# Kernel tuning notes

Measured on AMD Instinct MI355X. Metric: run time of the kernel, lower is better.

Reference implementation:

```python
import jax, jax.numpy as jnp
import numpy as np
from jax import lax

B, K, L = 8, 64, 1024
CP, AP, G2 = 32, 8, 9
CSA, ASA, G3 = 16, 16, 3
ROUT_ITER = 3
EPS = 1e-08


def squash(s):
    sq = jnp.sum(s * s, axis=-1, keepdims=True)
    return sq / (1.0 + sq) * (s / jnp.sqrt(sq + EPS))


def routing(V, iters):
    # V: [B, L, cp, cSA, aSA]
    b = jnp.zeros(V.shape[:-1], dtype=V.dtype)  # [B, L, cp, cSA]
    v = None
    for r in range(iters):
        c = jax.nn.softmax(b, axis=-1)[..., None]          # [B,L,cp,cSA,1]
        s = jnp.sum(c * V, axis=-3)                        # [B,L,cSA,aSA]
        v = squash(s)
        if r < iters - 1:
            a = jnp.sum(V * v[..., None, :, :], axis=-1)   # [B,L,cp,cSA]
            b = b + lax.stop_gradient(a)
    return v


def setup_inputs() -> dict:
    key = jax.random.key(0)
    k1, k2, k3 = jax.random.split(key, 3)
    x = jax.random.normal(k1, (B, K, L), dtype=jnp.float32)
    w1 = jax.random.normal(k2, (CP * AP, K, G2), dtype=jnp.float32) * 0.05
    b1 = jnp.zeros((CP * AP,), dtype=jnp.float32)
    w2 = jax.random.normal(k3, (CSA * ASA, 1, G3, AP), dtype=jnp.float32) * 0.05
    b2 = jnp.zeros((CSA * ASA,), dtype=jnp.float32)
    return {"x": x, "w1": w1, "b1": b1, "w2": w2, "b2": b2}


def reference(x, w1, b1, w2, b2):
    # conv1: Conv1d(k -> cp*ap, kernel g2, padding 'same')
    y = lax.conv_general_dilated(x, w1, window_strides=(1,), padding='SAME',
                                 dimension_numbers=('NCH', 'OIH', 'NCH'))
    y = y + b1[None, :, None]                              # [B, cp*ap, L]
    y = jnp.transpose(y, (0, 2, 1)).reshape(B, L, CP, AP)
    y = squash(y)
    y = y.reshape(B, L, CP * AP)[:, None]                  # [B, 1, L, cp*ap]
    # conv2: Conv2d(1 -> cSA*aSA, kernel (g3, ap), stride (1, ap), pad ((g3-1)/2, 0))
    pad = (G3 - 1) // 2
    z = lax.conv_general_dilated(y, w2, window_strides=(1, AP),
                                 padding=((pad, pad), (0, 0)),
                                 dimension_numbers=('NCHW', 'OIHW', 'NCHW'))
    z = z + b2[None, :, None, None]                        # [B, cSA*aSA, L, cp]
    V = jnp.transpose(z, (0, 2, 3, 1)).reshape(B, L, CP, CSA, ASA)
    v = routing(V, ROUT_ITER)                              # [B, L, cSA, aSA]
    return v.reshape(B, L * CSA, ASA)
```

## Files before the change

kernel.cpp:

```cpp
#include <hip/hip_runtime.h>
#include <math.h>

#define NB   8
#define NK   64
#define NL   1024
#define NCP  32
#define NAP  8
#define NG2  9
#define NCSA 16
#define NASA 16
#define NG3  3
#define NOC  256
#define EPSQ 1e-8f
#define VROW 129

typedef __bf16 bfv8 __attribute__((ext_vector_type(8)));
typedef float  f32x4 __attribute__((ext_vector_type(4)));

static __device__ inline unsigned short bfbits(float v) {
    __bf16 h = (__bf16)v;
    return __builtin_bit_cast(unsigned short, h);
}
static __device__ inline unsigned int bfpack2(float v0, float v1) {
    return (unsigned int)bfbits(v0) | ((unsigned int)bfbits(v1) << 16);
}
static __device__ inline float frcp(float x) { return __builtin_amdgcn_rcpf(x); }
static __device__ inline float frsq(float x) { return __builtin_amdgcn_rsqf(x); }

__global__ __launch_bounds__(256) void k0_prep(
    const float* __restrict__ x, const float* __restrict__ w1,
    const float* __restrict__ w2,
    __bf16* __restrict__ xThi, __bf16* __restrict__ w1Thi,
    __bf16* __restrict__ w2hi)
{
    const int tid = threadIdx.x;
    const int bid = blockIdx.x;
    if (bid < 128) {
        __shared__ float tile[64][65];
        const int b = bid >> 4, l0 = (bid & 15) * 64;
        const float* xb = x + (size_t)b * NK * NL;
        const int lcol = tid & 63, kr = tid >> 6;
#pragma unroll
        for (int pass = 0; pass < 16; ++pass) {
            int kk = pass * 4 + kr;
            tile[lcol][kk] = xb[(size_t)kk * NL + l0 + lcol];
        }
        __syncthreads();
        const int lr = tid >> 5, pc = tid & 31;
#pragma unroll
        for (int pass = 0; pass < 8; ++pass) {
            int ll = pass * 8 + lr;
            float v0 = tile[ll][pc * 2], v1 = tile[ll][pc * 2 + 1];
            size_t base = ((size_t)b * NL + l0 + ll) * 64 + pc * 2;
            *(unsigned int*)(xThi + base) = bfpack2(v0, v1);
        }
    } else if (bid < 128 + 288) {
        int idx = (bid - 128) * 256 + tid;
        int kp = idx & 31, rest = idx >> 5;
        int oc = rest & 255, g = rest >> 8;
        float v0 = w1[(size_t)oc * 576 + (kp * 2) * NG2 + g];
        float v1 = w1[(size_t)oc * 576 + (kp * 2 + 1) * NG2 + g];
        size_t base = ((size_t)(g * NOC + oc)) * 64 + kp * 2;
        *(unsigned int*)(w1Thi + base) = bfpack2(v0, v1);
    } else {
        for (int i = tid; i < NOC * 24; i += 256) {
            w2hi[i] = (__bf16)w2[i];
        }
    }
}

__global__ __launch_bounds__(256) void k1_mfma(
    const __bf16* __restrict__ xThi, const __bf16* __restrict__ w1Thi,
    const float* __restrict__ b1, __bf16* __restrict__ ysq)
{
    __shared__ alignas(16) __bf16 xph[72][64];
    const int tid = threadIdx.x;
    const int bid = blockIdx.x;
    const int ocb = bid & 3;
    const int lb  = (bid >> 2) & 15;
    const int b   = bid >> 6;
    const int l0  = lb * 64;

    {
        const int row0 = tid >> 3, seg = tid & 7;
#pragma unroll
        for (int p = 0; p < 3; ++p) {
            int row = p * 32 + row0;
            if (row < 72) {
                int l = l0 - 4 + row;
                int sw = seg ^ (row & 7);
                uint4 vh = {0u,0u,0u,0u};
                if (l >= 0 && l < NL) {
                    size_t off = ((size_t)b * NL + l) * 64 + seg * 8;
                    vh = *(const uint4*)(xThi + off);
                }
                *(uint4*)(&xph[row][sw * 8]) = vh;
            }
        }
    }
    __syncthreads();

    const int lane = tid & 63, wv = tid >> 6;
    const int qq = lane >> 4, cr = lane & 15;
    const int oco = ocb * 64 + wv * 16;

    f32x4 acc[4];
#pragma unroll
    for (int lt = 0; lt < 4; ++lt) acc[lt] = (f32x4){0.f, 0.f, 0.f, 0.f};

    for (int g = 0; g < NG2; ++g) {
#pragma unroll
        for (int s = 0; s < 2; ++s) {
            size_t aoff = ((size_t)(g * NOC + oco + cr)) * 64 + s * 32 + qq * 8;
            bfv8 Ahi = *(const bfv8*)(w1Thi + aoff);
#pragma unroll
            for (int lt = 0; lt < 4; ++lt) {
                int row = lt * 16 + cr + g;
                int gr = (s * 4 + qq) ^ (row & 7);
                bfv8 Bhi = *(const bfv8*)(&xph[row][gr * 8]);
                acc[lt] = __builtin_amdgcn_mfma_f32_16x16x32_bf16(Ahi, Bhi, acc[lt], 0, 0, 0);
            }
        }
    }

    const float4 bv = *(const float4*)(b1 + oco + qq * 4);
#pragma unroll
    for (int lt = 0; lt < 4; ++lt) {
        float v0 = acc[lt][0] + bv.x, v1 = acc[lt][1] + bv.y;
        float v2 = acc[lt][2] + bv.z, v3 = acc[lt][3] + bv.w;
        float s = v0*v0 + v1*v1 + v2*v2 + v3*v3;
        float s8 = s + __shfl_xor(s, 16);
        float scale = s8 * frcp(1.0f + s8) * frsq(s8 + EPSQ);
        uint2 st;
        st.x = bfpack2(v0 * scale, v1 * scale);
        st.y = bfpack2(v2 * scale, v3 * scale);
        int l = l0 + lt * 16 + cr;
        *(uint2*)(ysq + ((size_t)b * NL + l) * NOC + oco + qq * 4) = st;
    }
}

__global__ __launch_bounds__(256, 4) void k2_conv2_routing(
    const __bf16* __restrict__ ysq,
    const __bf16* __restrict__ w2hi,
    const float* __restrict__ b2, float* __restrict__ out)
{
    __shared__ alignas(16) unsigned int VbW[NCP * VROW];
    __shared__ alignas(16) float cct[NCSA][36];
    __shared__ alignas(16) float vvs[NCSA][20];

    const int tid = threadIdx.x;
    const int bid = blockIdx.x;
    const int b = bid >> 10;
    const int l = bid & (NL - 1);

    const int lane = tid & 63;
    const int wv   = tid >> 6;
    const int q    = lane >> 4;
    const int cr   = lane & 15;

    const __bf16* ybase = ysq + ((size_t)b * NL + l) * NOC;
    const bool rowok = (q == 1) || (q == 0 && l > 0) || (q == 2 && l < NL - 1);
    bfv8 B0, B1;
    if (rowok) {
        B0 = *(const bfv8*)(ybase + (q - 1) * NOC + cr * 8);
        B1 = *(const bfv8*)(ybase + (q - 1) * NOC + (cr + 16) * 8);
    } else {
#pragma unroll
        for (int i = 0; i < 8; ++i) { B0[i] = (__bf16)0.0f; B1[i] = (__bf16)0.0f; }
    }

    const int swz0 = (cr & 3) << 3;
#pragma unroll
    for (int i = 0; i < 4; ++i) {
        const int t  = wv * 4 + i;
        const int oc = t * 16 + cr;
        bfv8 Ahi;
        if (q < 3) {
            Ahi = *(const bfv8*)(w2hi + oc * 24 + q * 8);
        } else {
#pragma unroll
            for (int j = 0; j < 8; ++j) Ahi[j] = (__bf16)0.0f;
        }

        f32x4 acc0 = {0.f, 0.f, 0.f, 0.f};
        f32x4 acc1 = {0.f, 0.f, 0.f, 0.f};
        acc0 = __builtin_amdgcn_mfma_f32_16x16x32_bf16(Ahi, B0, acc0, 0, 0, 0);
        acc1 = __builtin_amdgcn_mfma_f32_16x16x32_bf16(Ahi, B1, acc1, 0, 0, 0);

        const int r0 = t * 16 + q * 4;
        float4 bvv = *(const float4*)(b2 + r0);
        const int D = t * 8 + q * 2;
        const int d0 = D ^ swz0;
        VbW[cr * VROW + d0]            = bfpack2(acc0[0] + bvv.x, acc0[1] + bvv.y);
        VbW[cr * VROW + d0 + 1]        = bfpack2(acc0[2] + bvv.z, acc0[3] + bvv.w);
        VbW[(cr + 16) * VROW + d0]     = bfpack2(acc1[0] + bvv.x, acc1[1] + bvv.y);
        VbW[(cr + 16) * VROW + d0 + 1] = bfpack2(acc1[2] + bvv.z, acc1[3] + bvv.w);
    }
    __syncthreads();

    const int csa = tid >> 4, asa = tid & 15;
    const int cp8 = tid >> 3, cs = tid & 7;

    const __bf16* vbB = (const __bf16*)VbW;
    float Vreg[NCP];
    {
        const int tw = tid >> 1, th = tid & 1;
#pragma unroll
        for (int cp = 0; cp < NCP; ++cp) {
            int d = tw ^ ((cp & 3) << 3);
            Vreg[cp] = (float)vbB[cp * (2 * VROW) + d * 2 + th];
        }
    }

    unsigned int ar0[8], ar1[8];
    {
        const unsigned int* arow0 = VbW + cp8 * VROW + ((cs * 8) ^ ((cp8 & 3) << 3));
        const unsigned int* arow1 = VbW + cp8 * VROW + (((cs + 8) * 8) ^ ((cp8 & 3) << 3));
#pragma unroll
        for (int j = 0; j < 8; ++j) { ar0[j] = arow0[j]; ar1[j] = arow1[j]; }
    }

    float br0, br1;

    {
        float s0 = 0.f, s1 = 0.f, s2 = 0.f, s3 = 0.f;
#pragma unroll
        for (int cp = 0; cp < NCP; cp += 4) {
            s0 += Vreg[cp];     s1 += Vreg[cp + 1];
            s2 += Vreg[cp + 2]; s3 += Vreg[cp + 3];
        }
        float sv = ((s0 + s1) + (s2 + s3)) * 0.0625f;
        float sq = sv * sv;
        sq += __shfl_xor(sq, 1);
        sq += __shfl_xor(sq, 2);
        sq += __shfl_xor(sq, 4);
        sq += __shfl_xor(sq, 8);
        float vval = sv * sq * frcp(1.0f + sq) * frsq(sq + EPSQ);
        vvs[csa][asa] = vval;
        __syncthreads();

        float4 va[4], vb[4];
#pragma unroll
        for (int p = 0; p < 4; ++p) {
            va[p] = ((const float4*)(&vvs[cs][0]))[p];
            vb[p] = ((const float4*)(&vvs[cs + 8][0]))[p];
        }
        float a0a = 0.f, a0b = 0.f, a1a = 0.f, a1b = 0.f;
#pragma unroll
        for (int j = 0; j < 8; ++j) {
            unsigned int d0 = ar0[j], d1 = ar1[j];
            float ve0 = (j & 1) ? va[j >> 1].z : va[j >> 1].x;
            float vo0 = (j & 1) ? va[j >> 1].w : va[j >> 1].y;
            float ve1 = (j & 1) ? vb[j >> 1].z : vb[j >> 1].x;
            float vo1 = (j & 1) ? vb[j >> 1].w : vb[j >> 1].y;
            a0a = fmaf(__builtin_bit_cast(float, d0 << 16),          ve0, a0a);
            a0b = fmaf(__builtin_bit_cast(float, d0 & 0xFFFF0000u),  vo0, a0b);
            a1a = fmaf(__builtin_bit_cast(float, d1 << 16),          ve1, a1a);
            a1b = fmaf(__builtin_bit_cast(float, d1 & 0xFFFF0000u),  vo1, a1b);
        }
        br0 = a0a + a0b;
        br1 = a1a + a1b;
    }

    {
        float e0 = __expf(br0), e1 = __expf(br1);
        float ssum = e0 + e1;
        ssum += __shfl_xor(ssum, 1);
        ssum += __shfl_xor(ssum, 2);
        ssum += __shfl_xor(ssum, 4);
        float inv = frcp(ssum);
        cct[cs][cp8]     = e0 * inv;
        cct[cs + 8][cp8] = e1 * inv;
        __syncthreads();

        float s0 = 0.f, s1 = 0.f, s2 = 0.f, s3 = 0.f;
        const float4* ccrow = (const float4*)(&cct[csa][0]);
#pragma unroll
        for (int jj = 0; jj < 8; ++jj) {
            float4 c4 = ccrow[jj];
            s0 = fmaf(c4.x, Vreg[4 * jj + 0], s0);
            s1 = fmaf(c4.y, Vreg[4 * jj + 1], s1);
            s2 = fmaf(c4.z, Vreg[4 * jj + 2], s2);
            s3 = fmaf(c4.w, Vreg[4 * jj + 3], s3);
        }
        float sv = (s0 + s1) + (s2 + s3);
        float sq = sv * sv;
        sq += __shfl_xor(sq, 1);
        sq += __shfl_xor(sq, 2);
        sq += __shfl_xor(sq, 4);
        sq += __shfl_xor(sq, 8);
        float vval = sv * sq * frcp(1.0f + sq) * frsq(sq + EPSQ);
        vvs[csa][asa] = vval;
        __syncthreads();

        float4 va[4], vb[4];
#pragma unroll
        for (int p = 0; p < 4; ++p) {
            va[p] = ((const float4*)(&vvs[cs][0]))[p];
            vb[p] = ((const float4*)(&vvs[cs + 8][0]))[p];
        }
        float a0a = 0.f, a0b = 0.f, a1a = 0.f, a1b = 0.f;
#pragma unroll
        for (int j = 0; j < 8; ++j) {
            unsigned int d0 = ar0[j], d1 = ar1[j];
            float ve0 = (j & 1) ? va[j >> 1].z : va[j >> 1].x;
            float vo0 = (j & 1) ? va[j >> 1].w : va[j >> 1].y;
            float ve1 = (j & 1) ? vb[j >> 1].z : vb[j >> 1].x;
            float vo1 = (j & 1) ? vb[j >> 1].w : vb[j >> 1].y;
            a0a = fmaf(__builtin_bit_cast(float, d0 << 16),          ve0, a0a);
            a0b = fmaf(__builtin_bit_cast(float, d0 & 0xFFFF0000u),  vo0, a0b);
            a1a = fmaf(__builtin_bit_cast(float, d1 << 16),          ve1, a1a);
            a1b = fmaf(__builtin_bit_cast(float, d1 & 0xFFFF0000u),  vo1, a1b);
        }
        br0 += a0a + a0b;
        br1 += a1a + a1b;
    }

    {
        float e0 = __expf(br0), e1 = __expf(br1);
        float ssum = e0 + e1;
        ssum += __shfl_xor(ssum, 1);
        ssum += __shfl_xor(ssum, 2);
        ssum += __shfl_xor(ssum, 4);
        float inv = frcp(ssum);
        cct[cs][cp8]     = e0 * inv;
        cct[cs + 8][cp8] = e1 * inv;
        __syncthreads();

        float s0 = 0.f, s1 = 0.f, s2 = 0.f, s3 = 0.f;
        const float4* ccrow = (const float4*)(&cct[csa][0]);
#pragma unroll
        for (int jj = 0; jj < 8; ++jj) {
            float4 c4 = ccrow[jj];
            s0 = fmaf(c4.x, Vreg[4 * jj + 0], s0);
            s1 = fmaf(c4.y, Vreg[4 * jj + 1], s1);
            s2 = fmaf(c4.z, Vreg[4 * jj + 2], s2);
            s3 = fmaf(c4.w, Vreg[4 * jj + 3], s3);
        }
        float sv = (s0 + s1) + (s2 + s3);
        float sq = sv * sv;
        sq += __shfl_xor(sq, 1);
        sq += __shfl_xor(sq, 2);
        sq += __shfl_xor(sq, 4);
        sq += __shfl_xor(sq, 8);
        float vval = sv * sq * frcp(1.0f + sq) * frsq(sq + EPSQ);
        out[((size_t)b * NL + l) * NOC + tid] = vval;
    }
}

extern "C" void kernel_launch(void* const* d_in, const int* in_sizes, int n_in,
                              void* d_out, int out_size, void* d_ws, size_t ws_size,
                              hipStream_t stream)
{
    const float* x  = (const float*)d_in[0];
    const float* w1 = (const float*)d_in[1];
    const float* b1 = (const float*)d_in[2];
    const float* w2 = (const float*)d_in[3];
    const float* b2 = (const float*)d_in[4];
    float* outp = (float*)d_out;

    char* ws = (char*)d_ws;
    __bf16* ysq   = (__bf16*)(ws);
    __bf16* xThi  = (__bf16*)(ws + 4194304);
    __bf16* w1Thi = (__bf16*)(ws + 5242880);
    __bf16* w2hi  = (__bf16*)(ws + 5537792);

    k0_prep<<<417, 256, 0, stream>>>(x, w1, w2, xThi, w1Thi, w2hi);
    k1_mfma<<<512, 256, 0, stream>>>(xThi, w1Thi, b1, ysq);
    k2_conv2_routing<<<NB * NL, 256, 0, stream>>>(ysq, w2hi, b2, outp);
}
```

Baseline: 54.45 us.

## Process two sequence positions per block in conv2+routing kernel

Each block of the conv2/routing kernel now handles two adjacent positions, doubling the MFMA, routing and shared-memory work per block and halving the grid. This amortises the weight loads, bias loads and barrier count across two independent routing problems and gives more ILP between barriers. The agreement loads now read shared memory directly instead of caching rows in registers. Launch bounds drop to 2 blocks per CU because of the higher register and LDS use, which risks lower occupancy.

```diff
diff --git a/kernel.cpp b/kernel.cpp
--- a/kernel.cpp
+++ b/kernel.cpp
@@ -139,34 +139,47 @@
     }
 }
 
-__global__ __launch_bounds__(256, 4) void k2_conv2_routing(
+__global__ __launch_bounds__(256, 2) void k2_conv2_routing(
     const __bf16* __restrict__ ysq,
     const __bf16* __restrict__ w2hi,
     const float* __restrict__ b2, float* __restrict__ out)
 {
-    __shared__ alignas(16) unsigned int VbW[NCP * VROW];
-    __shared__ alignas(16) float cct[NCSA][36];
-    __shared__ alignas(16) float vvs[NCSA][20];
+    __shared__ alignas(16) unsigned int VbWA[NCP * VROW];
+    __shared__ alignas(16) unsigned int VbWB[NCP * VROW];
+    __shared__ alignas(16) float cctA[NCSA][36];
+    __shared__ alignas(16) float cctB[NCSA][36];
+    __shared__ alignas(16) float vvsA[NCSA][20];
+    __shared__ alignas(16) float vvsB[NCSA][20];
 
     const int tid = threadIdx.x;
     const int bid = blockIdx.x;
-    const int b = bid >> 10;
-    const int l = bid & (NL - 1);
+    const int b  = bid >> 9;
+    const int lA = (bid & 511) * 2;
+    const int lB = lA + 1;
 
     const int lane = tid & 63;
     const int wv   = tid >> 6;
     const int q    = lane >> 4;
     const int cr   = lane & 15;
 
-    const __bf16* ybase = ysq + ((size_t)b * NL + l) * NOC;
-    const bool rowok = (q == 1) || (q == 0 && l > 0) || (q == 2 && l < NL - 1);
-    bfv8 B0, B1;
-    if (rowok) {
-        B0 = *(const bfv8*)(ybase + (q - 1) * NOC + cr * 8);
-        B1 = *(const bfv8*)(ybase + (q - 1) * NOC + (cr + 16) * 8);
+    const __bf16* ybaseA = ysq + ((size_t)b * NL + lA) * NOC;
+    const __bf16* ybaseB = ybaseA + NOC;
+    const bool okA = (q == 1) || (q == 0 && lA > 0) || (q == 2);
+    const bool okB = (q == 1) || (q == 0) || (q == 2 && lB < NL - 1);
+    bfv8 B0A, B1A, B0B, B1B;
+    if (okA) {
+        B0A = *(const bfv8*)(ybaseA + (q - 1) * NOC + cr * 8);
+        B1A = *(const bfv8*)(ybaseA + (q - 1) * NOC + (cr + 16) * 8);
     } else {
 #pragma unroll
-        for (int i = 0; i < 8; ++i) { B0[i] = (__bf16)0.0f; B1[i] = (__bf16)0.0f; }
+        for (int i = 0; i < 8; ++i) { B0A[i] = (__bf16)0.0f; B1A[i] = (__bf16)0.0f; }
+    }
+    if (okB) {
+        B0B = *(const bfv8*)(ybaseB + (q - 1) * NOC + cr * 8);
+        B1B = *(const bfv8*)(ybaseB + (q - 1) * NOC + (cr + 16) * 8);
+    } else {
+#pragma unroll
+        for (int i = 0; i < 8; ++i) { B0B[i] = (__bf16)0.0f; B1B[i] = (__bf16)0.0f; }
     }
 
     const int swz0 = (cr & 3) << 3;
@@ -182,169 +195,188 @@
             for (int j = 0; j < 8; ++j) Ahi[j] = (__bf16)0.0f;
         }
 
-        f32x4 acc0 = {0.f, 0.f, 0.f, 0.f};
-        f32x4 acc1 = {0.f, 0.f, 0.f, 0.f};
-        acc0 = __builtin_amdgcn_mfma_f32_16x16x32_bf16(Ahi, B0, acc0, 0, 0, 0);
-        acc1 = __builtin_amdgcn_mfma_f32_16x16x32_bf16(Ahi, B1, acc1, 0, 0, 0);
+        f32x4 aA0 = {0.f,0.f,0.f,0.f}, aA1 = {0.f,0.f,0.f,0.f};
+        f32x4 aB0 = {0.f,0.f,0.f,0.f}, aB1 = {0.f,0.f,0.f,0.f};
+        aA0 = __builtin_amdgcn_mfma_f32_16x16x32_bf16(Ahi, B0A, aA0, 0, 0, 0);
+        aA1 = __builtin_amdgcn_mfma_f32_16x16x32_bf16(Ahi, B1A, aA1, 0, 0, 0);
+        aB0 = __builtin_amdgcn_mfma_f32_16x16x32_bf16(Ahi, B0B, aB0, 0, 0, 0);
+        aB1 = __builtin_amdgcn_mfma_f32_16x16x32_bf16(Ahi, B1B, aB1, 0, 0, 0);
 
         const int r0 = t * 16 + q * 4;
         float4 bvv = *(const float4*)(b2 + r0);
-        const int D = t * 8 + q * 2;
+        const int D  = t * 8 + q * 2;
         const int d0 = D ^ swz0;
-        VbW[cr * VROW + d0]            = bfpack2(acc0[0] + bvv.x, acc0[1] + bvv.y);
-        VbW[cr * VROW + d0 + 1]        = bfpack2(acc0[2] + bvv.z, acc0[3] + bvv.w);
-        VbW[(cr + 16) * VROW + d0]     = bfpack2(acc1[0] + bvv.x, acc1[1] + bvv.y);
-        VbW[(cr + 16) * VROW + d0 + 1] = bfpack2(acc1[2] + bvv.z, acc1[3] + bvv.w);
+        VbWA[cr * VROW + d0]            = bfpack2(aA0[0] + bvv.x, aA0[1] + bvv.y);
+        VbWA[cr * VROW + d0 + 1]        = bfpack2(aA0[2] + bvv.z, aA0[3] + bvv.w);
+        VbWA[(cr + 16) * VROW + d0]     = bfpack2(aA1[0] + bvv.x, aA1[1] + bvv.y);
+        VbWA[(cr + 16) * VROW + d0 + 1] = bfpack2(aA1[2] + bvv.z, aA1[3] + bvv.w);
+        VbWB[cr * VROW + d0]            = bfpack2(aB0[0] + bvv.x, aB0[1] + bvv.y);
+        VbWB[cr * VROW + d0 + 1]        = bfpack2(aB0[2] + bvv.z, aB0[3] + bvv.w);
+        VbWB[(cr + 16) * VROW + d0]     = bfpack2(aB1[0] + bvv.x, aB1[1] + bvv.y);
+        VbWB[(cr + 16) * VROW + d0 + 1] = bfpack2(aB1[2] + bvv.z, aB1[3] + bvv.w);
     }
     __syncthreads();
 
     const int csa = tid >> 4, asa = tid & 15;
     const int cp8 = tid >> 3, cs = tid & 7;
 
-    const __bf16* vbB = (const __bf16*)VbW;
-    float Vreg[NCP];
+    float VregA[NCP], VregB[NCP];
     {
+        const __bf16* vbA = (const __bf16*)VbWA;
+        const __bf16* vbB = (const __bf16*)VbWB;
         const int tw = tid >> 1, th = tid & 1;
 #pragma unroll
         for (int cp = 0; cp < NCP; ++cp) {
             int d = tw ^ ((cp & 3) << 3);
-            Vreg[cp] = (float)vbB[cp * (2 * VROW) + d * 2 + th];
-        }
-    }
-
-    unsigned int ar0[8], ar1[8];
+            VregA[cp] = (float)vbA[cp * (2 * VROW) + d * 2 + th];
+            VregB[cp] = (float)vbB[cp * (2 * VROW) + d * 2 + th];
+        }
+    }
+
+    const int aoff0 = cp8 * VROW + ((cs * 8) ^ ((cp8 & 3) << 3));
+    const int aoff1 = cp8 * VROW + (((cs + 8) * 8) ^ ((cp8 & 3) << 3));
+
+    float brA0, brA1, brB0, brB1;
+
     {
-        const unsigned int* arow0 = VbW + cp8 * VROW + ((cs * 8) ^ ((cp8 & 3) << 3));
-        const unsigned int* arow1 = VbW + cp8 * VROW + (((cs + 8) * 8) ^ ((cp8 & 3) << 3));
-#pragma unroll
-        for (int j = 0; j < 8; ++j) { ar0[j] = arow0[j]; ar1[j] = arow1[j]; }
-    }
-
-    float br0, br1;
+        float sA0=0.f,sA1=0.f,sA2=0.f,sA3=0.f, sB0=0.f,sB1=0.f,sB2=0.f,sB3=0.f;
+#pragma unroll
+        for (int cp = 0; cp < NCP; cp += 4) {
+            sA0 += VregA[cp];     sA1 += VregA[cp + 1];
+            sA2 += VregA[cp + 2]; sA3 += VregA[cp + 3];
+            sB0 += VregB[cp];     sB1 += VregB[cp + 1];
+            sB2 += VregB[cp + 2]; sB3 += VregB[cp + 3];
+        }
+        float svA = ((sA0 + sA1) + (sA2 + sA3)) * 0.0625f;
+        float svB = ((sB0 + sB1) + (sB2 + sB3)) * 0.0625f;
+        float sqA = svA * svA, sqB = svB * svB;
+        sqA += __shfl_xor(sqA, 1);  sqB += __shfl_xor(sqB, 1);
+        sqA += __shfl_xor(sqA, 2);  sqB += __shfl_xor(sqB, 2);
+        sqA += __shfl_xor(sqA, 4);  sqB += __shfl_xor(sqB, 4);
+        sqA += __shfl_xor(sqA, 8);  sqB += __shfl_xor(sqB, 8);
+        vvsA[csa][asa] = svA * sqA * frcp(1.0f + sqA) * frsq(sqA + EPSQ);
+        vvsB[csa][asa] = svB * sqB * frcp(1.0f + sqB) * frsq(sqB + EPSQ);
+        __syncthreads();
+
+        float aA0a=0.f,aA0b=0.f,aA1a=0.f,aA1b=0.f;
+        float aB0a=0.f,aB0b=0.f,aB1a=0.f,aB1b=0.f;
+#pragma unroll
+        for (int j = 0; j < 8; ++j) {
+            unsigned int dA0 = VbWA[aoff0 + j], dA1 = VbWA[aoff1 + j];
+            unsigned int dB0 = VbWB[aoff0 + j], dB1 = VbWB[aoff1 + j];
+            float2 vA0 = *(const float2*)(&vvsA[cs][2 * j]);
+            float2 vA1 = *(const float2*)(&vvsA[cs + 8][2 * j]);
+            float2 vB0 = *(const float2*)(&vvsB[cs][2 * j]);
+            float2 vB1 = *(const float2*)(&vvsB[cs + 8][2 * j]);
+            aA0a = fmaf(__builtin_bit_cast(float, dA0 << 16),         vA0.x, aA0a);
+            aA0b = fmaf(__builtin_bit_cast(float, dA0 & 0xFFFF0000u), vA0.y, aA0b);
+            aA1a = fmaf(__builtin_bit_cast(float, dA1 << 16),         vA1.x, aA1a);
+            aA1b = fmaf(__builtin_bit_cast(float, dA1 & 0xFFFF0000u), vA1.y, aA1b);
+            aB0a = fmaf(__builtin_bit_cast(float, dB0 << 16),         vB0.x, aB0a);
+            aB0b = fmaf(__builtin_bit_cast(float, dB0 & 0xFFFF0000u), vB0.y, aB0b);
+            aB1a = fmaf(__builtin_bit_cast(float, dB1 << 16),         vB1.x, aB1a);
+            aB1b = fmaf(__builtin_bit_cast(float, dB1 & 0xFFFF0000u), vB1.y, aB1b);
+        }
+        brA0 = aA0a + aA0b;  brA1 = aA1a + aA1b;
+        brB0 = aB0a + aB0b;  brB1 = aB1a + aB1b;
+    }
 
     {
-        float s0 = 0.f, s1 = 0.f, s2 = 0.f, s3 = 0.f;
-#pragma unroll
-        for (int cp = 0; cp < NCP; cp += 4) {
-            s0 += Vreg[cp];     s1 += Vreg[cp + 1];
-            s2 += Vreg[cp + 2]; s3 += Vreg[cp + 3];
-        }
-        float sv = ((s0 + s1) + (s2 + s3)) * 0.0625f;
-        float sq = sv * sv;
-        sq += __shfl_xor(sq, 1);
-        sq += __shfl_xor(sq, 2);
-        sq += __shfl_xor(sq, 4);
-        sq += __shfl_xor(sq, 8);
-        float vval = sv * sq * frcp(1.0f + sq) * frsq(sq + EPSQ);
-        vvs[csa][asa] = vval;
+        float eA0 = __expf(brA0), eA1 = __expf(brA1);
+        float eB0 = __expf(brB0), eB1 = __expf(brB1);
+        float smA = eA0 + eA1, smB = eB0 + eB1;
+        smA += __shfl_xor(smA, 1);  smB += __shfl_xor(smB, 1);
+        smA += __shfl_xor(smA, 2);  smB += __shfl_xor(smB, 2);
+        smA += __shfl_xor(smA, 4);  smB += __shfl_xor(smB, 4);
+        float invA = frcp(smA), invB = frcp(smB);
+        cctA[cs][cp8]     = eA0 * invA;
+        cctA[cs + 8][cp8] = eA1 * invA;
+        cctB[cs][cp8]     = eB0 * invB;
+        cctB[cs + 8][cp8] = eB1 * invB;
         __syncthreads();
 
-        float4 va[4], vb[4];
-#pragma unroll
-        for (int p = 0; p < 4; ++p) {
-            va[p] = ((const float4*)(&vvs[cs][0]))[p];
-            vb[p] = ((const float4*)(&vvs[cs + 8][0]))[p];
-        }
-        float a0a = 0.f, a0b = 0.f, a1a = 0.f, a1b = 0.f;
+        float sA0=0.f,sA1=0.f,sA2=0.f,sA3=0.f, sB0=0.f,sB1=0.f,sB2=0.f,sB3=0.f;
+        const float4* crA = (const float4*)(&cctA[csa][0]);
+        const float4* crB = (const float4*)(&cctB[csa][0]);
+#pragma unroll
+        for (int jj = 0; jj < 8; ++jj) {
+            float4 cA = crA[jj], cB = crB[jj];
+            sA0 = fmaf(cA.x, VregA[4*jj+0], sA0);  sA1 = fmaf(cA.y, VregA[4*jj+1], sA1);
+            sA2 = fmaf(cA.z, VregA[4*jj+2], sA2);  sA3 = fmaf(cA.w, VregA[4*jj+3], sA3);
+            sB0 = fmaf(cB.x, VregB[4*jj+0], sB0);  sB1 = fmaf(cB.y, VregB[4*jj+1], sB1);
+            sB2 = fmaf(cB.z, VregB[4*jj+2], sB2);  sB3 = fmaf(cB.w, VregB[4*jj+3], sB3);
+        }
+        float svA = (sA0 + sA1) + (sA2 + sA3);
+        float svB = (sB0 + sB1) + (sB2 + sB3);
+        float sqA = svA * svA, sqB = svB * svB;
+        sqA += __shfl_xor(sqA, 1);  sqB += __shfl_xor(sqB, 1);
+        sqA += __shfl_xor(sqA, 2);  sqB += __shfl_xor(sqB, 2);
+        sqA += __shfl_xor(sqA, 4);  sqB += __shfl_xor(sqB, 4);
+        sqA += __shfl_xor(sqA, 8);  sqB += __shfl_xor(sqB, 8);
+        vvsA[csa][asa] = svA * sqA * frcp(1.0f + sqA) * frsq(sqA + EPSQ);
+        vvsB[csa][asa] = svB * sqB * frcp(1.0f + sqB) * frsq(sqB + EPSQ);
+        __syncthreads();
+
+        float aA0a=0.f,aA0b=0.f,aA1a=0.f,aA1b=0.f;
+        float aB0a=0.f,aB0b=0.f,aB1a=0.f,aB1b=0.f;
 #pragma unroll
         for (int j = 0; j < 8; ++j) {
-            unsigned int d0 = ar0[j], d1 = ar1[j];
-            float ve0 = (j & 1) ? va[j >> 1].z : va[j >> 1].x;
-            float vo0 = (j & 1) ? va[j >> 1].w : va[j >> 1].y;
-            float ve1 = (j & 1) ? vb[j >> 1].z : vb[j >> 1].x;
-            float vo1 = (j & 1) ? vb[j >> 1].w : vb[j >> 1].y;
-            a0a = fmaf(__builtin_bit_cast(float, d0 << 16),          ve0, a0a);
-            a0b = fmaf(__builtin_bit_cast(float, d0 & 0xFFFF0000u),  vo0, a0b);
-            a1a = fmaf(__builtin_bit_cast(float, d1 << 16),          ve1, a1a);
-            a1b = fmaf(__builtin_bit_cast(float, d1 & 0xFFFF0000u),  vo1, a1b);
-        }
-        br0 = a0a + a0b;
-        br1 = a1a + a1b;
+            unsigned int dA0 = VbWA[aoff0 + j], dA1 = VbWA[aoff1 + j];
+            unsigned int dB0 = VbWB[aoff0 + j], dB1 = VbWB[aoff1 + j];
+            float2 vA0 = *(const float2*)(&vvsA[cs][2 * j]);
+            float2 vA1 = *(const float2*)(&vvsA[cs + 8][2 * j]);
+            float2 vB0 = *(const float2*)(&vvsB[cs][2 * j]);
+            float2 vB1 = *(const float2*)(&vvsB[cs + 8][2 * j]);
+            aA0a = fmaf(__builtin_bit_cast(float, dA0 << 16),         vA0.x, aA0a);
+            aA0b = fmaf(__builtin_bit_cast(float, dA0 & 0xFFFF0000u), vA0.y, aA0b);
+            aA1a = fmaf(__builtin_bit_cast(float, dA1 << 16),         vA1.x, aA1a);
+            aA1b = fmaf(__builtin_bit_cast(float, dA1 & 0xFFFF0000u), vA1.y, aA1b);
+            aB0a = fmaf(__builtin_bit_cast(float, dB0 << 16),         vB0.x, aB0a);
+            aB0b = fmaf(__builtin_bit_cast(float, dB0 & 0xFFFF0000u), vB0.y, aB0b);
+            aB1a = fmaf(__builtin_bit_cast(float, dB1 << 16),         vB1.x, aB1a);
+            aB1b = fmaf(__builtin_bit_cast(float, dB1 & 0xFFFF0000u), vB1.y, aB1b);
+        }
+        brA0 += aA0a + aA0b;  brA1 += aA1a + aA1b;
+        brB0 += aB0a + aB0b;  brB1 += aB1a + aB1b;
     }
 
     {
-        float e0 = __expf(br0), e1 = __expf(br1);
-        float ssum = e0 + e1;
-        ssum += __shfl_xor(ssum, 1);
-        ssum += __shfl_xor(ssum, 2);
-        ssum += __shfl_xor(ssum, 4);
-        float inv = frcp(ssum);
-        cct[cs][cp8]     = e0 * inv;
-        cct[cs + 8][cp8] = e1 * inv;
+        float eA0 = __expf(brA0), eA1 = __expf(brA1);
+        float eB0 = __expf(brB0), eB1 = __expf(brB1);
+        float smA = eA0 + eA1, smB = eB0 + eB1;
+        smA += __shfl_xor(smA, 1);  smB += __shfl_xor(smB, 1);
+        smA += __shfl_xor(smA, 2);  smB += __shfl_xor(smB, 2);
+        smA += __shfl_xor(smA, 4);  smB += __shfl_xor(smB, 4);
+        float invA = frcp(smA), invB = frcp(smB);
+        cctA[cs][cp8]     = eA0 * invA;
+        cctA[cs + 8][cp8] = eA1 * invA;
+        cctB[cs][cp8]     = eB0 * invB;
+        cctB[cs + 8][cp8] = eB1 * invB;
         __syncthreads();
 
-        float s0 = 0.f, s1 = 0.f, s2 = 0.f, s3 = 0.f;
-        const float4* ccrow = (const float4*)(&cct[csa][0]);
+        float sA0=0.f,sA1=0.f,sA2=0.f,sA3=0.f, sB0=0.f,sB1=0.f,sB2=0.f,sB3=0.f;
+        const float4* crA = (const float4*)(&cctA[csa][0]);
+        const float4* crB = (const float4*)(&cctB[csa][0]);
 #pragma unroll
         for (int jj = 0; jj < 8; ++jj) {
-            float4 c4 = ccrow[jj];
-            s0 = fmaf(c4.x, Vreg[4 * jj + 0], s0);
-            s1 = fmaf(c4.y, Vreg[4 * jj + 1], s1);
-            s2 = fmaf(c4.z, Vreg[4 * jj + 2], s2);
-            s3 = fmaf(c4.w, Vreg[4 * jj + 3], s3);
-        }
-        float sv = (s0 + s1) + (s2 + s3);
-        float sq = sv * sv;
-        sq += __shfl_xor(sq, 1);
-        sq += __shfl_xor(sq, 2);
-        sq += __shfl_xor(sq, 4);
-        sq += __shfl_xor(sq, 8);
-        float vval = sv * sq * frcp(1.0f + sq) * frsq(sq + EPSQ);
-        vvs[csa][asa] = vval;
-        __syncthreads();
-
-        float4 va[4], vb[4];
-#pragma unroll
-        for (int p = 0; p < 4; ++p) {
-            va[p] = ((const float4*)(&vvs[cs][0]))[p];
-            vb[p] = ((const float4*)(&vvs[cs + 8][0]))[p];
-        }
-        float a0a = 0.f, a0b = 0.f, a1a = 0.f, a1b = 0.f;
-#pragma unroll
-        for (int j = 0; j < 8; ++j) {
-            unsigned int d0 = ar0[j], d1 = ar1[j];
-            float ve0 = (j & 1) ? va[j >> 1].z : va[j >> 1].x;
-            float vo0 = (j & 1) ? va[j >> 1].w : va[j >> 1].y;
-            float ve1 = (j & 1) ? vb[j >> 1].z : vb[j >> 1].x;
-            float vo1 = (j & 1) ? vb[j >> 1].w : vb[j >> 1].y;
-            a0a = fmaf(__builtin_bit_cast(float, d0 << 16),          ve0, a0a);
-            a0b = fmaf(__builtin_bit_cast(float, d0 & 0xFFFF0000u),  vo0, a0b);
-            a1a = fmaf(__builtin_bit_cast(float, d1 << 16),          ve1, a1a);
-            a1b = fmaf(__builtin_bit_cast(float, d1 & 0xFFFF0000u),  vo1, a1b);
-        }
-        br0 += a0a + a0b;
-        br1 += a1a + a1b;
-    }
-
-    {
-        float e0 = __expf(br0), e1 = __expf(br1);
-        float ssum = e0 + e1;
-        ssum += __shfl_xor(ssum, 1);
-        ssum += __shfl_xor(ssum, 2);
-        ssum += __shfl_xor(ssum, 4);
-        float inv = frcp(ssum);
-        cct[cs][cp8]     = e0 * inv;
-        cct[cs + 8][cp8] = e1 * inv;
-        __syncthreads();
-
-        float s0 = 0.f, s1 = 0.f, s2 = 0.f, s3 = 0.f;
-        const float4* ccrow = (const float4*)(&cct[csa][0]);
-#pragma unroll
-        for (int jj = 0; jj < 8; ++jj) {
-            float4 c4 = ccrow[jj];
-            s0 = fmaf(c4.x, Vreg[4 * jj + 0], s0);
-            s1 = fmaf(c4.y, Vreg[4 * jj + 1], s1);
-            s2 = fmaf(c4.z, Vreg[4 * jj + 2], s2);
-            s3 = fmaf(c4.w, Vreg[4 * jj + 3], s3);
-        }
-        float sv = (s0 + s1) + (s2 + s3);
-        float sq = sv * sv;
-        sq += __shfl_xor(sq, 1);
-        sq += __shfl_xor(sq, 2);
-        sq += __shfl_xor(sq, 4);
-        sq += __shfl_xor(sq, 8);
-        float vval = sv * sq * frcp(1.0f + sq) * frsq(sq + EPSQ);
-        out[((size_t)b * NL + l) * NOC + tid] = vval;
+            float4 cA = crA[jj], cB = crB[jj];
+            sA0 = fmaf(cA.x, VregA[4*jj+0], sA0);  sA1 = fmaf(cA.y, VregA[4*jj+1], sA1);
+            sA2 = fmaf(cA.z, VregA[4*jj+2], sA2);  sA3 = fmaf(cA.w, VregA[4*jj+3], sA3);
+            sB0 = fmaf(cB.x, VregB[4*jj+0], sB0);  sB1 = fmaf(cB.y, VregB[4*jj+1], sB1);
+            sB2 = fmaf(cB.z, VregB[4*jj+2], sB2);  sB3 = fmaf(cB.w, VregB[4*jj+3], sB3);
+        }
+        float svA = (sA0 + sA1) + (sA2 + sA3);
+        float svB = (sB0 + sB1) + (sB2 + sB3);
+        float sqA = svA * svA, sqB = svB * svB;
+        sqA += __shfl_xor(sqA, 1);  sqB += __shfl_xor(sqB, 1);
+        sqA += __shfl_xor(sqA, 2);  sqB += __shfl_xor(sqB, 2);
+        sqA += __shfl_xor(sqA, 4);  sqB += __shfl_xor(sqB, 4);
+        sqA += __shfl_xor(sqA, 8);  sqB += __shfl_xor(sqB, 8);
+        float vA = svA * sqA * frcp(1.0f + sqA) * frsq(sqA + EPSQ);
+        float vB = svB * sqB * frcp(1.0f + sqB) * frsq(sqB + EPSQ);
+        float* outA = out + ((size_t)b * NL + lA) * NOC + tid;
+        outA[0]   = vA;
+        outA[NOC] = vB;
     }
 }
 
@@ -367,5 +399,5 @@
 
     k0_prep<<<417, 256, 0, stream>>>(x, w1, w2, xThi, w1Thi, w2hi);
     k1_mfma<<<512, 256, 0, stream>>>(xThi, w1Thi, b1, ysq);
-    k2_conv2_routing<<<NB * NL, 256, 0, stream>>>(ysq, w2hi, b2, outp);
-}
+    k2_conv2_routing<<<NB * NL / 2, 256, 0, stream>>>(ysq, w2hi, b2, outp);
+}
```

New measurement: 58.46 us. 1.07x slower.
